# Performance work log

Measured on AMD Instinct MI355X. Metric: run time of the kernel, lower is better.

## Reference

```python
import jax, jax.numpy as jnp
import numpy as np

D_STATE = 16
D_CONV = 4
EXPAND = 2
DT_RANK = 2  # ceil(d_model/16) for d_model=32
GROUPS = 4
EPS = 1e-5


def setup_inputs() -> dict:
    key = jax.random.key(0)
    ks = jax.random.split(key, 10)
    C = 32
    d_in = EXPAND * C  # 64
    B, H, W = 2, 256, 256
    s = 0.02
    x = jax.random.normal(ks[0], (B, C, H, W), jnp.float32)
    W_in = jax.random.normal(ks[1], (C, 2 * d_in), jnp.float32) * s
    conv_w = jax.random.normal(ks[2], (d_in, D_CONV), jnp.float32) * 0.3
    conv_b = jnp.zeros((d_in,), jnp.float32)
    W_xproj = jax.random.normal(ks[3], (d_in, DT_RANK + 2 * D_STATE), jnp.float32) * s
    W_dt = jax.random.normal(ks[4], (DT_RANK, d_in), jnp.float32) * (DT_RANK ** -0.5)
    b_dt = jnp.full((d_in,), -3.0, jnp.float32)  # softplus(-3) ~ 0.05 dt init
    A_log = jnp.log(jnp.tile(jnp.arange(1.0, D_STATE + 1.0, dtype=jnp.float32), (d_in, 1)))
    Dp = jnp.ones((d_in,), jnp.float32)
    W_out = jax.random.normal(ks[5], (d_in, C), jnp.float32) * s
    gn_gamma = jnp.ones((C,), jnp.float32)
    gn_beta = jnp.zeros((C,), jnp.float32)
    return {"x": x, "W_in": W_in, "conv_w": conv_w, "conv_b": conv_b,
            "W_xproj": W_xproj, "W_dt": W_dt, "b_dt": b_dt, "A_log": A_log,
            "Dp": Dp, "W_out": W_out, "gn_gamma": gn_gamma, "gn_beta": gn_beta}


def reference(x, W_in, conv_w, conv_b, W_xproj, W_dt, b_dt, A_log, Dp, W_out, gn_gamma, gn_beta):
    B, C, H, W = x.shape
    d_in = W_in.shape[1] // 2
    L = B * H * W
    # [B,C,H,W] -> [B,H,W,C] -> [L,C] (batch folded into sequence, as in source)
    xf = jnp.transpose(x, (0, 2, 3, 1)).reshape(L, C)
    xz = xf @ W_in                       # [L, 2*d_in]
    u, z = xz[:, :d_in], xz[:, d_in:]
    # causal depthwise conv1d, kernel D_CONV, padding D_CONV-1, truncated to L
    up = jnp.pad(u, ((D_CONV - 1, 0), (0, 0)))
    uc = conv_b
    for k in range(D_CONV):
        uc = uc + up[k:k + L] * conv_w[:, k]
    uc = uc * jax.nn.sigmoid(uc)         # SiLU
    dbc = uc @ W_xproj                   # [L, dt_rank + 2*d_state]
    dt = dbc[:, :DT_RANK]
    Bm = dbc[:, DT_RANK:DT_RANK + D_STATE]   # [L, d_state]
    Cm = dbc[:, DT_RANK + D_STATE:]          # [L, d_state]
    delta = jax.nn.softplus(dt @ W_dt + b_dt)  # [L, d_in]
    A = -jnp.exp(A_log)                  # [d_in, d_state]

    def step(h, inp):
        d_t, B_t, C_t, u_t = inp
        h = jnp.exp(d_t[:, None] * A) * h + (d_t * u_t)[:, None] * B_t[None, :]
        return h, (h * C_t[None, :]).sum(-1)

    h0 = jnp.zeros((d_in, D_STATE), xf.dtype)
    _, ys = jax.lax.scan(step, h0, (delta, Bm, Cm, uc))  # ys: [L, d_in]
    y = ys + Dp * uc
    y = y * (z * jax.nn.sigmoid(z))      # gate with SiLU(z)
    out = (y @ W_out).reshape(B, H, W, C).transpose(0, 3, 1, 2)  # [B,C,H,W]
    # GroupNorm(4, C) + SiLU
    g = out.reshape(B, GROUPS, C // GROUPS, H, W)
    mu = g.mean((2, 3, 4), keepdims=True)
    var = g.var((2, 3, 4), keepdims=True)
    g = (g - mu) * jax.lax.rsqrt(var + EPS)
    out = g.reshape(B, C, H, W) * gn_gamma[None, :, None, None] + gn_beta[None, :, None, None]
    out = out * jax.nn.sigmoid(out)
    return out + x
```

## Files before the change

### kernel.cpp

```cpp
#include <hip/hip_runtime.h>

#define L_TOT   131072
#define HW      65536
#define CCH     32
#define DIN     64
#define NCHUNK  4096
#define TCH     32
#define NGRP    128
#define GCH     32
#define NBLK    (L_TOT/64)


typedef short bf16x8 __attribute__((ext_vector_type(8)));
typedef float f32x4  __attribute__((ext_vector_type(4)));
typedef unsigned short u16x8 __attribute__((ext_vector_type(8)));

__device__ __forceinline__ float sigmoidf_(float x){ return 1.0f/(1.0f + __expf(-x)); }

__device__ __forceinline__ unsigned short f2bf(float f){
    union { float f; unsigned int u; } v; v.f = f;
    unsigned int u = v.u;
    return (unsigned short)((u + 0x7fffu + ((u >> 16) & 1u)) >> 16);
}
__device__ __forceinline__ float bf2f(unsigned short s){
    union { unsigned int u; float f; } v; v.u = ((unsigned int)s) << 16;
    return v.f;
}

__global__ void __launch_bounds__(256)
k_halo(const float* __restrict__ x, const float* __restrict__ W_in,
       float* __restrict__ u_halo){
    int tid = blockIdx.x*256 + threadIdx.x;
    int j  = tid & 63;
    int bh = tid >> 6;
    int b  = bh / 3;
    int hi = bh - b*3;
    float acc = 0.f;
    if (b > 0){
        int token = b*64 - 3 + hi;
        const float* xp = x + ((size_t)(token >> 16))*CCH*HW + (size_t)(token & (HW-1));
        #pragma unroll
        for (int c=0;c<CCH;c++)
            acc = fmaf(xp[(size_t)c*HW], W_in[c*2*DIN + j], acc);
    }
    u_halo[tid] = acc;
}

#define OFF_US   0
#define OFF_WIN  4556
#define OFF_OUT  7116
#define OFF_WXT  9420
#define LDS_FLOATS 11148

__global__ void __launch_bounds__(256)
k_front(const float* __restrict__ x, const float* __restrict__ W_in,
        const float* __restrict__ conv_w, const float* __restrict__ conv_b,
        const float* __restrict__ W_xproj, const float* __restrict__ W_dt,
        const float* __restrict__ b_dt, const float* __restrict__ u_halo,
        float* __restrict__ z, float* __restrict__ uc,
        float* __restrict__ delta, float* __restrict__ Bm, float* __restrict__ Cm,
        float* __restrict__ S, float* __restrict__ sd){
    __shared__ float lds[LDS_FLOATS];
    unsigned short* Wb = (unsigned short*)(lds + OFF_WIN);
    unsigned short* Xb = (unsigned short*)(lds + OFF_OUT);
    unsigned short* Wx = (unsigned short*)(lds + OFF_WXT);
    unsigned short* Ub = (unsigned short*)(lds + OFF_WIN);
    const int tid  = threadIdx.x;
    const int w    = tid >> 6;
    const int lane = tid & 63;
    const int base = blockIdx.x * 64;

    #pragma unroll
    for (int it=0; it<16; it++){
        int c = it*2 + (tid>>7);
        int j = tid & 127;
        Wb[j*40 + c] = f2bf(W_in[c*128 + j]);
    }
    {
        int c  = tid >> 3;
        int t8 = (tid & 7) * 8;
        const float* xp = x + (size_t)(base >> 16)*CCH*HW + (base & (HW-1)) + (size_t)c*HW + t8;
        float4 v0 = ((const float4*)xp)[0];
        float4 v1 = ((const float4*)xp)[1];
        float xs[8] = {v0.x,v0.y,v0.z,v0.w, v1.x,v1.y,v1.z,v1.w};
        #pragma unroll
        for (int i=0;i<8;i++) Xb[(t8+i)*40 + c] = f2bf(xs[i]);
    }
    #pragma unroll
    for (int it=0; it<9; it++){
        int f = it*256 + tid;
        if (f < 2176){
            int dd = f / 34;
            int mm = f - dd*34;
            Wx[mm*72 + dd] = f2bf(W_xproj[f]);
        }
    }
    {
        unsigned int* Wxu = (unsigned int*)Wx;
        if (tid < 252){ Wxu[1224 + tid] = 0u; Wxu[1224 + 252 + tid] = 0u; }
    }
    if (tid < 192)
        lds[OFF_US + (tid>>6)*68 + (tid&63)] = u_halo[blockIdx.x*192 + tid];
    __syncthreads();

    {
        const int j0w = w*32;
        bf16x8 af[4];
        #pragma unroll
        for (int tt=0; tt<4; tt++)
            af[tt] = *reinterpret_cast<const bf16x8*>(&Xb[(tt*16 + (lane&15))*40 + (lane>>4)*8]);
        f32x4 acc[4][2];
        #pragma unroll
        for (int tt=0; tt<4; tt++){ acc[tt][0]=(f32x4)0.f; acc[tt][1]=(f32x4)0.f; }
        #pragma unroll
        for (int jt=0; jt<2; jt++){
            bf16x8 bfr = *reinterpret_cast<const bf16x8*>(&Wb[(j0w + jt*16 + (lane&15))*40 + (lane>>4)*8]);
            #pragma unroll
            for (int tt=0; tt<4; tt++)
                acc[tt][jt] = __builtin_amdgcn_mfma_f32_16x16x32_bf16(af[tt], bfr, acc[tt][jt], 0, 0, 0);
        }
        if (w < 2){
            #pragma unroll
            for (int tt=0; tt<4; tt++)
                #pragma unroll
                for (int jt=0; jt<2; jt++){
                    int j = j0w + jt*16 + (lane&15);
                    #pragma unroll
                    for (int r=0;r<4;r++){
                        int t = tt*16 + (lane>>4)*4 + r;
                        lds[OFF_US + (t+3)*68 + j] = acc[tt][jt][r];
                    }
                }
        } else {
            #pragma unroll
            for (int tt=0; tt<4; tt++)
                #pragma unroll
                for (int jt=0; jt<2; jt++){
                    int j = j0w - 64 + jt*16 + (lane&15);
                    #pragma unroll
                    for (int r=0;r<4;r++){
                        int t = tt*16 + (lane>>4)*4 + r;
                        z[(size_t)(base+t)*DIN + j] = acc[tt][jt][r];
                    }
                }
        }
    }
    __syncthreads();

    {
        int d = lane;
        float4 cwv = reinterpret_cast<const float4*>(conv_w)[d];
        float  cb  = conv_b[d];
        #pragma unroll
        for (int i=0;i<16;i++){
            int tl = w*16 + i;
            float v = cb;
            v = fmaf(lds[OFF_US + (tl+0)*68 + d], cwv.x, v);
            v = fmaf(lds[OFF_US + (tl+1)*68 + d], cwv.y, v);
            v = fmaf(lds[OFF_US + (tl+2)*68 + d], cwv.z, v);
            v = fmaf(lds[OFF_US + (tl+3)*68 + d], cwv.w, v);
            v = v * sigmoidf_(v);
            unsigned short us = f2bf(v);
            uc[(size_t)(base + tl)*DIN + d] = bf2f(us);
            Ub[tl*72 + d] = us;
        }
    }
    __syncthreads();

    {
        f32x4 acc3[3];
        acc3[0]=(f32x4)0.f; acc3[1]=(f32x4)0.f; acc3[2]=(f32x4)0.f;
        #pragma unroll
        for (int k=0; k<2; k++){
            bf16x8 au = *reinterpret_cast<const bf16x8*>(&Ub[(w*16 + (lane&15))*72 + k*32 + (lane>>4)*8]);
            #pragma unroll
            for (int mt=0; mt<3; mt++){
                bf16x8 bw = *reinterpret_cast<const bf16x8*>(&Wx[(mt*16 + (lane&15))*72 + k*32 + (lane>>4)*8]);
                acc3[mt] = __builtin_amdgcn_mfma_f32_16x16x32_bf16(au, bw, acc3[mt], 0, 0, 0);
            }
        }
        __syncthreads();
        #pragma unroll
        for (int mt=0; mt<3; mt++){
            int m = mt*16 + (lane&15);
            if (m < 34){
                int col = (m < 2) ? m : m + 2;
                #pragma unroll
                for (int r=0;r<4;r++){
                    int t = w*16 + (lane>>4)*4 + r;
                    lds[OFF_OUT + t*36 + col] = acc3[mt][r];
                }
            }
        }
    }
    __syncthreads();

    {
        int dd = lane;
        float wdt0 = W_dt[dd], wdt1 = W_dt[DIN+dd], bdd = b_dt[dd];
        #pragma unroll
        for (int it=0; it<16; it++){
            int t = it*4 + w;
            float dt0 = lds[OFF_OUT + t*36 + 0];
            float dt1 = lds[OFF_OUT + t*36 + 1];
            float pre = fmaf(dt0, wdt0, fmaf(dt1, wdt1, bdd));
            float v = (pre > 20.f) ? pre : __logf(1.f + __expf(pre));
            delta[(size_t)(base + t)*DIN + dd] = v;
            lds[OFF_US + t*68 + dd] = v;
        }
        {
            int t = tid >> 2, q = tid & 3;
            float4 vb = *reinterpret_cast<const float4*>(&lds[OFF_OUT + t*36 + 4  + q*4]);
            float4 vc = *reinterpret_cast<const float4*>(&lds[OFF_OUT + t*36 + 20 + q*4]);
            *reinterpret_cast<float4*>(Bm + (size_t)(base+t)*16 + q*4) = vb;
            *reinterpret_cast<float4*>(Cm + (size_t)(base+t)*16 + q*4) = vc;
        }
    }
    __syncthreads();

    {
        int c  = tid >> 7;
        int hh = (tid >> 6) & 1;
        int d  = tid & 63;
        float h8[8];
        #pragma unroll
        for (int k=0;k<8;k++) h8[k]=0.f;
        float sdl = 0.f;
        #pragma unroll 4
        for (int tt=0; tt<TCH; tt++){
            int tl = c*32 + tt;
            float dl = lds[OFF_US + tl*68 + d];
            float uu = bf2f(Ub[tl*72 + d]);
            float4 bq0 = *reinterpret_cast<const float4*>(&lds[OFF_OUT + tl*36 + 4 + hh*8]);
            float4 bq1 = *reinterpret_cast<const float4*>(&lds[OFF_OUT + tl*36 + 8 + hh*8]);
            float bbv[8] = {bq0.x,bq0.y,bq0.z,bq0.w, bq1.x,bq1.y,bq1.z,bq1.w};
            float e1 = __expf(-dl);
            float e2 = e1*e1, e4 = e2*e2, e8 = e4*e4;
            float aa = hh ? (e8*e1) : e1;
            float du = dl*uu;
            sdl += dl;
            #pragma unroll
            for (int k=0;k<8;k++){
                h8[k] = fmaf(aa, h8[k], du*bbv[k]);
                aa *= e1;
            }
        }
        int chunk = blockIdx.x*2 + c;
        float4* So = (float4*)(S + (size_t)chunk*1024 + d*16 + hh*8);
        So[0] = make_float4(h8[0],h8[1],h8[2],h8[3]);
        So[1] = make_float4(h8[4],h8[5],h8[6],h8[7]);
        if (hh == 0) sd[chunk*64 + d] = sdl;
    }
}

__global__ void k_scan2a(float* __restrict__ S, float* __restrict__ sd,
                         float* __restrict__ Sg, float* __restrict__ sdg){
    int gt = blockIdx.x*blockDim.x + threadIdx.x;
    int g  = gt >> 10;
    int e  = gt & 1023;
    int d  = e >> 4;
    float f = (float)((e & 15) + 1);
    float ps = 0.f, s = 0.f;
    for (int i=0;i<GCH;i++){
        int chunk = g*GCH + i;
        size_t idx = (size_t)chunk*1024 + e;
        float sc  = S[idx];
        float sdc = sd[chunk*64 + d];
        S[idx] = s;
        if ((e & 15) == 0) sd[chunk*64 + d] = ps;
        float pc = __expf(-sdc * f);
        s = fmaf(s, pc, sc);
        ps += sdc;
    }
    Sg[g*1024 + e] = s;
    if ((e & 15) == 0) sdg[g*64 + d] = ps;
}

__global__ void k_scan2b(const float* __restrict__ Sg, const float* __restrict__ sdg,
                         float* __restrict__ Hg){
    int e = threadIdx.x;
    int d = e >> 4;
    float f = (float)((e & 15) + 1);
    float h = 0.f;
    for (int g=0; g<NGRP; g++){
        Hg[g*1024 + e] = h;
        float pg = __expf(-sdg[g*64 + d] * f);
        h = fmaf(pg, h, Sg[g*1024 + e]);
    }
}

__global__ void __launch_bounds__(256)
k_back(const float* __restrict__ delta, const float* __restrict__ uc,
       const float* __restrict__ Bm, const float* __restrict__ Cm,
       const float* __restrict__ z,
       const float* __restrict__ S, const float* __restrict__ sd,
       const float* __restrict__ Hg, const float* __restrict__ Dp,
       const float* __restrict__ W_out,
       float* __restrict__ o, float* __restrict__ stats){
    __shared__ unsigned short ysb[128*72];
    __shared__ float red[2][8];
    int tid  = threadIdx.x;
    int wid  = tid >> 6;
    int d    = tid & 63;
    int chunk = blockIdx.x*4 + wid;
    int g = chunk >> 5;

    float h[16];
    {
        size_t sbase = (size_t)chunk*1024 + d*16;
        float psdl = sd[chunk*64 + d];
        const float* Hr = Hg + (size_t)g*1024 + d*16;
        #pragma unroll
        for (int n=0;n<16;n++){
            float pex = __expf(-psdl * (float)(n+1));
            h[n] = fmaf(pex, Hr[n], S[sbase + n]);
        }
    }
    float Dpd = Dp[d];
    int t0 = chunk*TCH;
    const float* dp = delta + (size_t)t0*DIN + d;
    const float* up = uc    + (size_t)t0*DIN + d;
    const float* zp = z     + (size_t)t0*DIN + d;
    const float4* B4 = (const float4*)(Bm + (size_t)t0*16);
    const float4* C4 = (const float4*)(Cm + (size_t)t0*16);

    float  ndl = dp[0], nuu = up[0], nzz = zp[0];
    float4 nb0=B4[0], nb1=B4[1], nb2=B4[2], nb3=B4[3];
    float4 nc0=C4[0], nc1=C4[1], nc2=C4[2], nc3=C4[3];

    for (int tt=0; tt<TCH; tt++){
        float dl=ndl, uu=nuu, zz=nzz;
        float4 b0=nb0,b1=nb1,b2=nb2,b3=nb3;
        float4 c0=nc0,c1=nc1,c2=nc2,c3=nc3;
        if (tt+1 < TCH){
            ndl = dp[(size_t)(tt+1)*DIN]; nuu = up[(size_t)(tt+1)*DIN]; nzz = zp[(size_t)(tt+1)*DIN];
            nb0 = B4[(tt+1)*4+0]; nb1 = B4[(tt+1)*4+1]; nb2 = B4[(tt+1)*4+2]; nb3 = B4[(tt+1)*4+3];
            nc0 = C4[(tt+1)*4+0]; nc1 = C4[(tt+1)*4+1]; nc2 = C4[(tt+1)*4+2]; nc3 = C4[(tt+1)*4+3];
        }
        float bb[16] = {b0.x,b0.y,b0.z,b0.w, b1.x,b1.y,b1.z,b1.w,
                        b2.x,b2.y,b2.z,b2.w, b3.x,b3.y,b3.z,b3.w};
        float cc[16] = {c0.x,c0.y,c0.z,c0.w, c1.x,c1.y,c1.z,c1.w,
                        c2.x,c2.y,c2.z,c2.w, c3.x,c3.y,c3.z,c3.w};
        float e1 = __expf(-dl);
        float e2 = e1*e1;
        float a[16];
        a[0]=e1; a[1]=e2;
        #pragma unroll
        for (int n=2;n<16;n++) a[n] = a[n-2]*e2;
        float du = dl*uu;
        float yv = 0.f;
        #pragma unroll
        for (int n=0;n<16;n++){
            h[n] = fmaf(a[n], h[n], du*bb[n]);
            yv   = fmaf(h[n], cc[n], yv);
        }
        yv = fmaf(Dpd, uu, yv);
        yv *= zz * sigmoidf_(zz);
        ysb[(wid*32 + tt)*72 + d] = f2bf(yv);
    }
    __syncthreads();

    if (tid < 128){
        int tl = tid;
        int t  = blockIdx.x*128 + tl;
        float acc[CCH];
        #pragma unroll
        for (int j=0;j<CCH;j++) acc[j]=0.f;
        #pragma unroll
        for (int q8=0; q8<8; q8++){
            u16x8 v8 = *reinterpret_cast<const u16x8*>(&ysb[tl*72 + q8*8]);
            #pragma unroll
            for (int r=0;r<8;r++){
                int dd = q8*8 + r;
                float yd = bf2f(v8[r]);
                #pragma unroll
                for (int j=0;j<CCH;j++) acc[j] = fmaf(yd, W_out[dd*CCH+j], acc[j]);
            }
        }
        float4* o4 = (float4*)(o + (size_t)t*CCH);
        #pragma unroll
        for (int q=0;q<CCH/4;q++) o4[q] = make_float4(acc[4*q],acc[4*q+1],acc[4*q+2],acc[4*q+3]);

        int wv = tl >> 6;
        #pragma unroll
        for (int gg=0; gg<4; gg++){
            float s = 0.f, q2 = 0.f;
            #pragma unroll
            for (int r=0;r<8;r++){ float v = acc[gg*8+r]; s += v; q2 = fmaf(v,v,q2); }
            #pragma unroll
            for (int off=32; off>0; off>>=1){
                s  += __shfl_down(s,  off);
                q2 += __shfl_down(q2, off);
            }
            if ((tl & 63) == 0){ red[wv][gg*2] = s; red[wv][gg*2+1] = q2; }
        }
    }
    __syncthreads();
    if (tid < 8){
        int b = (blockIdx.x*128) >> 16;
        float s = red[0][tid] + red[1][tid];
        atomicAdd(&stats[b*8 + tid], s);
    }
}

__global__ void k_final(const float* __restrict__ o, const float* __restrict__ x,
                        const float* __restrict__ stats, const float* __restrict__ gn_gamma,
                        const float* __restrict__ gn_beta, float* __restrict__ out){
    int t  = blockIdx.x*blockDim.x + threadIdx.x;
    int b  = t >> 16;
    int hw = t & (HW-1);
    float mu[4], rs[4];
    #pragma unroll
    for (int gg=0; gg<4; gg++){
        float sm = stats[b*8+gg*2], sq = stats[b*8+gg*2+1];
        const float invN = 1.f/524288.f;
        float m = sm*invN;
        float var = fmaf(sq, invN, -m*m);
        mu[gg]=m; rs[gg]=rsqrtf(var + 1e-5f);
    }
    const float4* o4 = (const float4*)(o + (size_t)t*CCH);
    const float* xb = x + (size_t)b*CCH*HW + hw;
    float* ob = out + (size_t)b*CCH*HW + hw;
    #pragma unroll
    for (int q=0;q<CCH/4;q++){
        float4 v = o4[q];
        float vv[4] = {v.x, v.y, v.z, v.w};
        #pragma unroll
        for (int r=0;r<4;r++){
            int j = 4*q+r;
            int gg = j >> 3;
            float val = fmaf((vv[r]-mu[gg])*rs[gg], gn_gamma[j], gn_beta[j]);
            val = val * sigmoidf_(val);
            ob[(size_t)j*HW] = val + xb[(size_t)j*HW];
        }
    }
}

extern "C" void kernel_launch(void* const* d_in, const int* in_sizes, int n_in,
                              void* d_out, int out_size, void* d_ws, size_t ws_size,
                              hipStream_t stream) {
    const float* x       = (const float*)d_in[0];
    const float* W_in    = (const float*)d_in[1];
    const float* conv_w  = (const float*)d_in[2];
    const float* conv_b  = (const float*)d_in[3];
    const float* W_xproj = (const float*)d_in[4];
    const float* W_dt    = (const float*)d_in[5];
    const float* b_dt    = (const float*)d_in[6];
    const float* Dp      = (const float*)d_in[8];
    const float* W_out   = (const float*)d_in[9];
    const float* gn_gamma= (const float*)d_in[10];
    const float* gn_beta = (const float*)d_in[11];
    float* out = (float*)d_out;

    const size_t N_LD = (size_t)L_TOT * DIN;
    float* w     = (float*)d_ws;
    float* z     = w;
    float* uc    = z + N_LD;
    float* delta = uc + N_LD;
    float* Bm    = delta + N_LD;
    float* Cm    = Bm + (size_t)L_TOT*16;
    float* S     = Cm + (size_t)L_TOT*16;
    float* sd    = S  + (size_t)NCHUNK*1024;
    float* Sg    = sd + (size_t)NCHUNK*64;
    float* sdg   = Sg + (size_t)NGRP*1024;
    float* Hg    = sdg+ (size_t)NGRP*64;
    float* stats = Hg + (size_t)NGRP*1024;
    float* o     = stats + 16;
    float* u_halo= o + (size_t)L_TOT*CCH;

    hipMemsetAsync(stats, 0, 16*sizeof(float), stream);

    k_halo  <<<(NBLK*3*64)/256, 256, 0, stream>>>(x, W_in, u_halo);
    k_front <<<NBLK, 256, 0, stream>>>(x, W_in, conv_w, conv_b, W_xproj, W_dt, b_dt,
                                       u_halo, z, uc, delta, Bm, Cm, S, sd);
    k_scan2a<<<(NGRP*1024)/256, 256, 0, stream>>>(S, sd, Sg, sdg);
    k_scan2b<<<1, 1024, 0, stream>>>(Sg, sdg, Hg);
    k_back  <<<NCHUNK/4, 256, 0, stream>>>(delta, uc, Bm, Cm, z, S, sd, Hg, Dp, W_out,
                                           o, stats);
    k_final <<<L_TOT/256, 256, 0, stream>>>(o, x, stats, gn_gamma, gn_beta, out);
}
```

Before: 157.2 us.

## Halve scan chunk length, store conv output as bf16, reuse halo buffer

Scan chunks shrink from 32 to 16 timesteps, so each thread in the front kernel holds all 16 state entries for one chunk and k_back launches twice as many blocks, each handling 64 timesteps. The SiLU-conv output uc is written and read as bf16 instead of fp32, which halves that global stream. The u_halo buffer now aliases the o buffer, and the block-level stats reduction is replaced by per-wave atomics. The aim is shorter serial scan chains with more parallelism and less memory traffic, at the cost of more chunk-state writes, more scan2a work and more atomics.

Measured after the change: 351.2 us. 123% more time.

```diff
diff --git a/kernel.cpp b/kernel.cpp
--- a/kernel.cpp
+++ b/kernel.cpp
@@ -4,10 +4,10 @@
 #define HW      65536
 #define CCH     32
 #define DIN     64
-#define NCHUNK  4096
-#define TCH     32
+#define NCHUNK  8192
+#define TCH     16
 #define NGRP    128
-#define GCH     32
+#define GCH     64
 #define NBLK    (L_TOT/64)
 
 
@@ -57,7 +57,7 @@
         const float* __restrict__ conv_w, const float* __restrict__ conv_b,
         const float* __restrict__ W_xproj, const float* __restrict__ W_dt,
         const float* __restrict__ b_dt, const float* __restrict__ u_halo,
-        float* __restrict__ z, float* __restrict__ uc,
+        float* __restrict__ z, unsigned short* __restrict__ ucb,
         float* __restrict__ delta, float* __restrict__ Bm, float* __restrict__ Cm,
         float* __restrict__ S, float* __restrict__ sd){
     __shared__ float lds[LDS_FLOATS];
@@ -161,7 +161,7 @@
             v = fmaf(lds[OFF_US + (tl+3)*68 + d], cwv.w, v);
             v = v * sigmoidf_(v);
             unsigned short us = f2bf(v);
-            uc[(size_t)(base + tl)*DIN + d] = bf2f(us);
+            ucb[(size_t)(base + tl)*DIN + d] = us;
             Ub[tl*72 + d] = us;
         }
     }
@@ -219,37 +219,41 @@
     __syncthreads();
 
     {
-        int c  = tid >> 7;
-        int hh = (tid >> 6) & 1;
-        int d  = tid & 63;
-        float h8[8];
-        #pragma unroll
-        for (int k=0;k<8;k++) h8[k]=0.f;
+        int c = tid >> 6;
+        int d = tid & 63;
+        float h16[16];
+        #pragma unroll
+        for (int n=0;n<16;n++) h16[n]=0.f;
         float sdl = 0.f;
         #pragma unroll 4
         for (int tt=0; tt<TCH; tt++){
-            int tl = c*32 + tt;
+            int tl = c*TCH + tt;
             float dl = lds[OFF_US + tl*68 + d];
             float uu = bf2f(Ub[tl*72 + d]);
-            float4 bq0 = *reinterpret_cast<const float4*>(&lds[OFF_OUT + tl*36 + 4 + hh*8]);
-            float4 bq1 = *reinterpret_cast<const float4*>(&lds[OFF_OUT + tl*36 + 8 + hh*8]);
-            float bbv[8] = {bq0.x,bq0.y,bq0.z,bq0.w, bq1.x,bq1.y,bq1.z,bq1.w};
+            float4 bq0 = *reinterpret_cast<const float4*>(&lds[OFF_OUT + tl*36 + 4]);
+            float4 bq1 = *reinterpret_cast<const float4*>(&lds[OFF_OUT + tl*36 + 8]);
+            float4 bq2 = *reinterpret_cast<const float4*>(&lds[OFF_OUT + tl*36 + 12]);
+            float4 bq3 = *reinterpret_cast<const float4*>(&lds[OFF_OUT + tl*36 + 16]);
+            float bbv[16] = {bq0.x,bq0.y,bq0.z,bq0.w, bq1.x,bq1.y,bq1.z,bq1.w,
+                             bq2.x,bq2.y,bq2.z,bq2.w, bq3.x,bq3.y,bq3.z,bq3.w};
             float e1 = __expf(-dl);
-            float e2 = e1*e1, e4 = e2*e2, e8 = e4*e4;
-            float aa = hh ? (e8*e1) : e1;
+            float e2 = e1*e1;
+            float a[16];
+            a[0]=e1; a[1]=e2;
+            #pragma unroll
+            for (int n=2;n<16;n++) a[n] = a[n-2]*e2;
             float du = dl*uu;
             sdl += dl;
             #pragma unroll
-            for (int k=0;k<8;k++){
-                h8[k] = fmaf(aa, h8[k], du*bbv[k]);
-                aa *= e1;
-            }
-        }
-        int chunk = blockIdx.x*2 + c;
-        float4* So = (float4*)(S + (size_t)chunk*1024 + d*16 + hh*8);
-        So[0] = make_float4(h8[0],h8[1],h8[2],h8[3]);
-        So[1] = make_float4(h8[4],h8[5],h8[6],h8[7]);
-        if (hh == 0) sd[chunk*64 + d] = sdl;
+            for (int n=0;n<16;n++) h16[n] = fmaf(a[n], h16[n], du*bbv[n]);
+        }
+        int chunk = blockIdx.x*4 + c;
+        float4* So = (float4*)(S + (size_t)chunk*1024 + d*16);
+        So[0] = make_float4(h16[0],h16[1],h16[2],h16[3]);
+        So[1] = make_float4(h16[4],h16[5],h16[6],h16[7]);
+        So[2] = make_float4(h16[8],h16[9],h16[10],h16[11]);
+        So[3] = make_float4(h16[12],h16[13],h16[14],h16[15]);
+        sd[chunk*64 + d] = sdl;
     }
 }
 
@@ -290,20 +294,19 @@
 }
 
 __global__ void __launch_bounds__(256)
-k_back(const float* __restrict__ delta, const float* __restrict__ uc,
+k_back(const float* __restrict__ delta, const unsigned short* __restrict__ ucb,
        const float* __restrict__ Bm, const float* __restrict__ Cm,
        const float* __restrict__ z,
        const float* __restrict__ S, const float* __restrict__ sd,
        const float* __restrict__ Hg, const float* __restrict__ Dp,
        const float* __restrict__ W_out,
        float* __restrict__ o, float* __restrict__ stats){
-    __shared__ unsigned short ysb[128*72];
-    __shared__ float red[2][8];
+    __shared__ unsigned short ysb[64*72];
     int tid  = threadIdx.x;
     int wid  = tid >> 6;
     int d    = tid & 63;
     int chunk = blockIdx.x*4 + wid;
-    int g = chunk >> 5;
+    int g = chunk >> 6;
 
     float h[16];
     {
@@ -319,12 +322,12 @@
     float Dpd = Dp[d];
     int t0 = chunk*TCH;
     const float* dp = delta + (size_t)t0*DIN + d;
-    const float* up = uc    + (size_t)t0*DIN + d;
+    const unsigned short* up = ucb + (size_t)t0*DIN + d;
     const float* zp = z     + (size_t)t0*DIN + d;
     const float4* B4 = (const float4*)(Bm + (size_t)t0*16);
     const float4* C4 = (const float4*)(Cm + (size_t)t0*16);
 
-    float  ndl = dp[0], nuu = up[0], nzz = zp[0];
+    float  ndl = dp[0], nuu = bf2f(up[0]), nzz = zp[0];
     float4 nb0=B4[0], nb1=B4[1], nb2=B4[2], nb3=B4[3];
     float4 nc0=C4[0], nc1=C4[1], nc2=C4[2], nc3=C4[3];
 
@@ -333,7 +336,7 @@
         float4 b0=nb0,b1=nb1,b2=nb2,b3=nb3;
         float4 c0=nc0,c1=nc1,c2=nc2,c3=nc3;
         if (tt+1 < TCH){
-            ndl = dp[(size_t)(tt+1)*DIN]; nuu = up[(size_t)(tt+1)*DIN]; nzz = zp[(size_t)(tt+1)*DIN];
+            ndl = dp[(size_t)(tt+1)*DIN]; nuu = bf2f(up[(size_t)(tt+1)*DIN]); nzz = zp[(size_t)(tt+1)*DIN];
             nb0 = B4[(tt+1)*4+0]; nb1 = B4[(tt+1)*4+1]; nb2 = B4[(tt+1)*4+2]; nb3 = B4[(tt+1)*4+3];
             nc0 = C4[(tt+1)*4+0]; nc1 = C4[(tt+1)*4+1]; nc2 = C4[(tt+1)*4+2]; nc3 = C4[(tt+1)*4+3];
         }
@@ -356,13 +359,13 @@
         }
         yv = fmaf(Dpd, uu, yv);
         yv *= zz * sigmoidf_(zz);
-        ysb[(wid*32 + tt)*72 + d] = f2bf(yv);
-    }
-    __syncthreads();
-
-    if (tid < 128){
+        ysb[(wid*TCH + tt)*72 + d] = f2bf(yv);
+    }
+    __syncthreads();
+
+    if (tid < 64){
         int tl = tid;
-        int t  = blockIdx.x*128 + tl;
+        int t  = blockIdx.x*64 + tl;
         float acc[CCH];
         #pragma unroll
         for (int j=0;j<CCH;j++) acc[j]=0.f;
@@ -381,7 +384,7 @@
         #pragma unroll
         for (int q=0;q<CCH/4;q++) o4[q] = make_float4(acc[4*q],acc[4*q+1],acc[4*q+2],acc[4*q+3]);
 
-        int wv = tl >> 6;
+        int b = (blockIdx.x*64) >> 16;
         #pragma unroll
         for (int gg=0; gg<4; gg++){
             float s = 0.f, q2 = 0.f;
@@ -392,14 +395,11 @@
                 s  += __shfl_down(s,  off);
                 q2 += __shfl_down(q2, off);
             }
-            if ((tl & 63) == 0){ red[wv][gg*2] = s; red[wv][gg*2+1] = q2; }
-        }
-    }
-    __syncthreads();
-    if (tid < 8){
-        int b = (blockIdx.x*128) >> 16;
-        float s = red[0][tid] + red[1][tid];
-        atomicAdd(&stats[b*8 + tid], s);
+            if (tid == 0){
+                atomicAdd(&stats[b*8 + gg*2 + 0], s);
+                atomicAdd(&stats[b*8 + gg*2 + 1], q2);
+            }
+        }
     }
 }
 
@@ -455,8 +455,8 @@
     const size_t N_LD = (size_t)L_TOT * DIN;
     float* w     = (float*)d_ws;
     float* z     = w;
-    float* uc    = z + N_LD;
-    float* delta = uc + N_LD;
+    unsigned short* ucb = (unsigned short*)(z + N_LD);
+    float* delta = z + N_LD + N_LD/2;
     float* Bm    = delta + N_LD;
     float* Cm    = Bm + (size_t)L_TOT*16;
     float* S     = Cm + (size_t)L_TOT*16;
@@ -466,16 +466,16 @@
     float* Hg    = sdg+ (size_t)NGRP*64;
     float* stats = Hg + (size_t)NGRP*1024;
     float* o     = stats + 16;
-    float* u_halo= o + (size_t)L_TOT*CCH;
+    float* u_halo= o;
 
     hipMemsetAsync(stats, 0, 16*sizeof(float), stream);
 
     k_halo  <<<(NBLK*3*64)/256, 256, 0, stream>>>(x, W_in, u_halo);
     k_front <<<NBLK, 256, 0, stream>>>(x, W_in, conv_w, conv_b, W_xproj, W_dt, b_dt,
-                                       u_halo, z, uc, delta, Bm, Cm, S, sd);
+                                       u_halo, z, ucb, delta, Bm, Cm, S, sd);
     k_scan2a<<<(NGRP*1024)/256, 256, 0, stream>>>(S, sd, Sg, sdg);
     k_scan2b<<<1, 1024, 0, stream>>>(Sg, sdg, Hg);
-    k_back  <<<NCHUNK/4, 256, 0, stream>>>(delta, uc, Bm, Cm, z, S, sd, Hg, Dp, W_out,
+    k_back  <<<NCHUNK/4, 256, 0, stream>>>(delta, ucb, Bm, Cm, z, S, sd, Hg, Dp, W_out,
                                            o, stats);
     k_final <<<L_TOT/256, 256, 0, stream>>>(o, x, stats, gn_gamma, gn_beta, out);
 }
```
